# Kernel tuning notes

Hardware: AMD Instinct MI355X
Metric: run time of the kernel (lower is better)

The kernel has to match this reference:

```python
import jax, jax.numpy as jnp
import numpy as np

EPS_DIV = 1e-6    # safe_div clamp
EPS_NORM = 1e-12  # F.normalize eps
EPS_PD = 1e-6     # F.pairwise_distance eps (added to the difference)


def setup_inputs() -> dict:
    key = jax.random.key(0)
    k1, k2, k3 = jax.random.split(key, 3)
    B, N, D, C = 8, 2048, 512, 8192
    x = jax.random.normal(k1, (B, N, D), dtype=jnp.float32)
    W = jax.random.normal(k2, (D, D), dtype=jnp.float32) * (1.0 / np.sqrt(D))
    codebook = jax.random.normal(k3, (C, D), dtype=jnp.float32)
    return {"x": x, "W": W, "codebook": codebook}


def reference(x, W, codebook):
    sg = jax.lax.stop_gradient
    # implicit codebook = Linear(dim, dim, bias=False)(codebook)  -> codebook @ W^T
    imp = codebook @ W.T                                  # [C, D]

    lead = x.shape[:-1]
    D = x.shape[-1]
    xf = x.reshape(-1, D)                                 # [T, D]

    # nearest-neighbor search (no_grad in original): squared-dist argmin == cdist argmin
    d2 = (jnp.sum(xf * xf, axis=-1, keepdims=True)
          - 2.0 * (xf @ imp.T)
          + jnp.sum(imp * imp, axis=-1)[None, :])         # [T, C]
    indices = jnp.argmin(sg(d2), axis=-1)                 # [T]

    qf = imp[indices]                                     # [T, D] gather

    # commit loss: (pairwise_distance(x, q.detach())**2).mean(); torch adds eps to the diff
    diff = xf - sg(qf) + EPS_PD
    commit_loss = jnp.mean(jnp.sum(diff * diff, axis=-1))

    # rotation trick
    norm_x = jnp.linalg.norm(xf, axis=-1, keepdims=True)  # [T, 1]
    norm_q = jnp.linalg.norm(qf, axis=-1, keepdims=True)
    u = xf / jnp.maximum(norm_x, EPS_DIV)
    q = qf / jnp.maximum(norm_q, EPS_DIV)
    s = u + q
    w = sg(s / jnp.maximum(jnp.linalg.norm(s, axis=-1, keepdims=True), EPS_NORM))
    e = xf
    # e - 2 (e.w) w + 2 (e.u_sg) q_sg   (rank-1 products per row)
    rot = (e
           - 2.0 * jnp.sum(e * w, axis=-1, keepdims=True) * w
           + 2.0 * jnp.sum(e * sg(u), axis=-1, keepdims=True) * sg(q))
    quantized = rot * sg(norm_q / jnp.maximum(norm_x, EPS_DIV))

    quantized = quantized.reshape(*lead, D)
    indices = indices.reshape(*lead)
    return quantized, indices, commit_loss
```

## Files before the change

### kernel.cpp

```cpp
#include <hip/hip_runtime.h>
#include <cstdint>
#include <cstddef>

#define DD 512
#define TT 16384
#define CC 8192
#define SPLITC 64
#define EPS_DIV 1e-6f
#define EPS_NORM 1e-12f
#define EPS_PD 1e-6f

typedef _Float16 half8 __attribute__((ext_vector_type(8)));
typedef _Float16 half4 __attribute__((ext_vector_type(4)));
typedef float floatx4 __attribute__((ext_vector_type(4)));

#define GLDS16(g, l) __builtin_amdgcn_global_load_lds( \
    (const __attribute__((address_space(1))) void*)(g), \
    (__attribute__((address_space(3))) void*)(l), 16, 0, 0)

__global__ __launch_bounds__(128) void k_split(const float* __restrict__ src,
                                               _Float16* __restrict__ dst) {
  const int row = blockIdx.x;
  const int col = threadIdx.x * 4;
  float4 v = *(const float4*)(src + (size_t)row * DD + col);
  half4 h, l;
  h.x = (_Float16)v.x; l.x = (_Float16)(v.x - (float)h.x);
  h.y = (_Float16)v.y; l.y = (_Float16)(v.y - (float)h.y);
  h.z = (_Float16)v.z; l.z = (_Float16)(v.z - (float)h.z);
  h.w = (_Float16)v.w; l.w = (_Float16)(v.w - (float)h.w);
  *(half4*)(dst + (size_t)row * 1024 + col) = h;
  *(half4*)(dst + (size_t)row * 1024 + 512 + col) = l;
}

__global__ __launch_bounds__(128) void k_cast16(const float* __restrict__ src,
                                                _Float16* __restrict__ dst) {
  const int row = blockIdx.x;
  const int col = threadIdx.x * 4;
  float4 v = *(const float4*)(src + (size_t)row * DD + col);
  half4 h;
  h.x = (_Float16)v.x; h.y = (_Float16)v.y;
  h.z = (_Float16)v.z; h.w = (_Float16)v.w;
  *(half4*)(dst + (size_t)row * DD + col) = h;
}

__global__ __launch_bounds__(256) void k_gemm_mfma(
    const _Float16* __restrict__ cbs, const _Float16* __restrict__ Ws,
    float* __restrict__ imp, _Float16* __restrict__ ih) {
  __shared__ __align__(16) char smem[65536];
  const int tid = threadIdx.x;
  const int w = tid >> 6, lane = tid & 63;
  const int quad = lane >> 4, l15 = lane & 15;
  const int wm = (w & 1) * 64, wn = (w >> 1) * 64;
  const int c0 = blockIdx.x * 128;
  const int n0 = blockIdx.y * 128;

  const int srow8 = lane >> 3;
  const int scol = ((lane & 7) ^ srow8) << 3;
  size_t arow[4], brow[4];
#pragma unroll
  for (int j = 0; j < 4; ++j) {
    arow[j] = (size_t)(c0 + j * 32 + w * 8 + srow8) * 1024 + scol;
    brow[j] = (size_t)(n0 + j * 32 + w * 8 + srow8) * 1024 + scol;
  }
  int aoff[4], boff[4];
#pragma unroll
  for (int i = 0; i < 4; ++i) {
    aoff[i] = ((wm + i * 16 + l15) * 64 + ((quad ^ (l15 & 7)) << 3)) * 2;
    boff[i] = ((wn + i * 16 + l15) * 64 + ((quad ^ (l15 & 7)) << 3)) * 2;
  }

  auto stage = [&](int buf, int ak, int bk) {
    char* ab = smem + buf * 32768;
    char* bb = ab + 16384;
#pragma unroll
    for (int j = 0; j < 4; ++j) {
      GLDS16(cbs + arow[j] + ak, (_Float16*)ab + (j * 32 + w * 8) * 64);
      GLDS16(Ws  + brow[j] + bk, (_Float16*)bb + (j * 32 + w * 8) * 64);
    }
  };

  floatx4 acc[4][4] = {};
  stage(0, 0, 0);
#pragma unroll 2
  for (int it = 0; it < 24; ++it) {
    __syncthreads();
    if (it < 23) {
      const int n = it + 1;
      const int p = n >> 3, kk = n & 7;
      const int ak = ((p == 2) ? 512 : 0) + kk * 64;
      const int bk = ((p == 1) ? 512 : 0) + kk * 64;
      stage(n & 1, ak, bk);
    }
    const char* ab = smem + (it & 1) * 32768;
    const char* bb = ab + 16384;
#pragma unroll
    for (int ks = 0; ks < 2; ++ks) {
      const int kx = ks * 64;
      half8 a[4], b[4];
#pragma unroll
      for (int mi = 0; mi < 4; ++mi)
        a[mi] = *(const half8*)(ab + (aoff[mi] ^ kx));
#pragma unroll
      for (int ni = 0; ni < 4; ++ni)
        b[ni] = *(const half8*)(bb + (boff[ni] ^ kx));
#pragma unroll
      for (int mi = 0; mi < 4; ++mi)
#pragma unroll
        for (int ni = 0; ni < 4; ++ni)
          acc[mi][ni] = __builtin_amdgcn_mfma_f32_16x16x32_f16(
              a[mi], b[ni], acc[mi][ni], 0, 0, 0);
    }
  }
#pragma unroll
  for (int mi = 0; mi < 4; ++mi)
#pragma unroll
    for (int r = 0; r < 4; ++r) {
      const int c = c0 + wm + mi * 16 + quad * 4 + r;
#pragma unroll
      for (int ni = 0; ni < 4; ++ni) {
        const int d = n0 + wn + ni * 16 + l15;
        const float v = acc[mi][ni][r];
        imp[(size_t)c * DD + d] = v;
        ih[(size_t)c * DD + d] = (_Float16)v;
      }
    }
}

__global__ __launch_bounds__(256) void k_row_norm2(
    const float* __restrict__ imp, float* __restrict__ cnorm) {
  const int lane = threadIdx.x & 63;
  const int row = blockIdx.x * 4 + (threadIdx.x >> 6);
  const float* p = imp + (size_t)row * DD + lane * 8;
  float4 a = *(const float4*)p;
  float4 b = *(const float4*)(p + 4);
  float s = a.x * a.x + a.y * a.y + a.z * a.z + a.w * a.w +
            b.x * b.x + b.y * b.y + b.z * b.z + b.w * b.w;
#pragma unroll
  for (int m = 1; m < 64; m <<= 1) s += __shfl_xor(s, m);
  if (lane == 0) cnorm[row] = s;
}

__global__ __launch_bounds__(256) void k_dist_top2(
    const _Float16* __restrict__ xh, const _Float16* __restrict__ ih,
    const float* __restrict__ cnorm,
    float* __restrict__ bval, int* __restrict__ bidx) {
  __shared__ __align__(16) char smem[65536];
  const int tid = threadIdx.x;
  const int w = tid >> 6, lane = tid & 63;
  const int quad = lane >> 4, l15 = lane & 15;
  const int wm = (w & 1) * 64, wn = (w >> 1) * 64;
  const int r0 = blockIdx.x * 128;
  const int c0 = blockIdx.y * 128;

  const int srow8 = lane >> 3;
  const int scol = ((lane & 7) ^ srow8) << 3;
  size_t arow[4], brow[4];
#pragma unroll
  for (int j = 0; j < 4; ++j) {
    arow[j] = (size_t)(r0 + j * 32 + w * 8 + srow8) * DD + scol;
    brow[j] = (size_t)(c0 + j * 32 + w * 8 + srow8) * DD + scol;
  }
  int aoff[4], boff[4];
#pragma unroll
  for (int i = 0; i < 4; ++i) {
    aoff[i] = ((wm + i * 16 + l15) * 64 + ((quad ^ (l15 & 7)) << 3)) * 2;
    boff[i] = ((wn + i * 16 + l15) * 64 + ((quad ^ (l15 & 7)) << 3)) * 2;
  }

  auto stage = [&](int buf, int k0) {
    char* ab = smem + buf * 32768;
    char* bb = ab + 16384;
#pragma unroll
    for (int j = 0; j < 4; ++j) {
      GLDS16(xh + arow[j] + k0, (_Float16*)ab + (j * 32 + w * 8) * 64);
      GLDS16(ih + brow[j] + k0, (_Float16*)bb + (j * 32 + w * 8) * 64);
    }
  };

  floatx4 acc[4][4] = {};
  stage(0, 0);
#pragma unroll
  for (int kk = 0; kk < 8; ++kk) {
    __syncthreads();
    if (kk < 7) stage((kk + 1) & 1, (kk + 1) * 64);
    const char* ab = smem + (kk & 1) * 32768;
    const char* bb = ab + 16384;
#pragma unroll
    for (int ks = 0; ks < 2; ++ks) {
      const int kx = ks * 64;
      half8 a[4], b[4];
#pragma unroll
      for (int mi = 0; mi < 4; ++mi)
        a[mi] = *(const half8*)(ab + (aoff[mi] ^ kx));
#pragma unroll
      for (int ni = 0; ni < 4; ++ni)
        b[ni] = *(const half8*)(bb + (boff[ni] ^ kx));
#pragma unroll
      for (int mi = 0; mi < 4; ++mi)
#pragma unroll
        for (int ni = 0; ni < 4; ++ni)
          acc[mi][ni] = __builtin_amdgcn_mfma_f32_16x16x32_f16(
              a[mi], b[ni], acc[mi][ni], 0, 0, 0);
    }
  }
  float best[16];
  int bsti[16];
#pragma unroll
  for (int mi = 0; mi < 4; ++mi)
#pragma unroll
    for (int r = 0; r < 4; ++r) {
      const int s = mi * 4 + r;
      best[s] = 3.4e38f; bsti[s] = 0;
#pragma unroll
      for (int ni = 0; ni < 4; ++ni) {
        const int c = c0 + wn + ni * 16 + l15;
        const float v = fmaf(-2.0f, acc[mi][ni][r], cnorm[c]);
        if (v < best[s]) { best[s] = v; bsti[s] = c; }
      }
    }
  __syncthreads();
  float* rv = (float*)smem;
  int* ri = (int*)(smem + 16896);
  const int e = (w >> 1) * 16 + l15;
#pragma unroll
  for (int mi = 0; mi < 4; ++mi)
#pragma unroll
    for (int r = 0; r < 4; ++r) {
      const int row = wm + mi * 16 + quad * 4 + r;
      rv[row * 33 + e] = best[mi * 4 + r];
      ri[row * 33 + e] = bsti[mi * 4 + r];
    }
  __syncthreads();
  if (tid < 128) {
    float v1 = 3.4e38f, v2 = 3.4e38f;
    int i1 = 0x7fffffff, i2 = 0x7fffffff;
#pragma unroll
    for (int t = 0; t < 32; ++t) {
      const float v = rv[tid * 33 + t];
      const int i = ri[tid * 33 + t];
      if (v < v1 || (v == v1 && i < i1)) {
        v2 = v1; i2 = i1; v1 = v; i1 = i;
      } else if (v < v2 || (v == v2 && i < i2)) {
        v2 = v; i2 = i;
      }
    }
    const size_t o = ((size_t)blockIdx.y * TT + r0 + tid) * 2;
    bval[o] = v1; bval[o + 1] = v2;
    bidx[o] = i1; bidx[o + 1] = i2;
  }
}

__global__ __launch_bounds__(256) void k_epilogue(
    const float* __restrict__ x, const float* __restrict__ imp,
    const float* __restrict__ cnorm,
    const float* __restrict__ bval, const int* __restrict__ bidx,
    float* __restrict__ outq, float* __restrict__ outidx,
    float* __restrict__ rloss) {
  const int lane = threadIdx.x & 63;
  const int row = blockIdx.x * 4 + (threadIdx.x >> 6);
  const size_t o = ((size_t)lane * TT + row) * 2;
  float v1 = bval[o], v2 = bval[o + 1];
  int i1 = bidx[o], i2 = bidx[o + 1];
#pragma unroll
  for (int m = 1; m < 64; m <<= 1) {
    const float w1 = __shfl_xor(v1, m), w2 = __shfl_xor(v2, m);
    const int j1 = __shfl_xor(i1, m), j2 = __shfl_xor(i2, m);
    if (w1 < v1 || (w1 == v1 && j1 < i1)) {
      if (v1 < w2 || (v1 == w2 && i1 < j2)) { v2 = v1; i2 = i1; }
      else { v2 = w2; i2 = j2; }
      v1 = w1; i1 = j1;
    } else {
      if (w1 < v2 || (w1 == v2 && j1 < i2)) { v2 = w1; i2 = j1; }
    }
  }
  const float* xr = x + (size_t)row * DD + lane * 8;
  float e[8], qa[8], qb[8];
  *(float4*)&e[0] = *(const float4*)xr;
  *(float4*)&e[4] = *(const float4*)(xr + 4);
  const float* q1p = imp + (size_t)i1 * DD + lane * 8;
  const float* q2p = imp + (size_t)i2 * DD + lane * 8;
  *(float4*)&qa[0] = *(const float4*)q1p;
  *(float4*)&qa[4] = *(const float4*)(q1p + 4);
  *(float4*)&qb[0] = *(const float4*)q2p;
  *(float4*)&qb[4] = *(const float4*)(q2p + 4);
  float d1 = 0.f, d2 = 0.f;
#pragma unroll
  for (int k = 0; k < 8; ++k) {
    d1 = fmaf(e[k], qa[k], d1);
    d2 = fmaf(e[k], qb[k], d2);
  }
#pragma unroll
  for (int m = 1; m < 64; m <<= 1) {
    d1 += __shfl_xor(d1, m);
    d2 += __shfl_xor(d2, m);
  }
  const float s1 = fmaf(-2.0f, d1, cnorm[i1]);
  const float s2 = fmaf(-2.0f, d2, cnorm[i2]);
  const bool use2 = (s2 < s1) || (s2 == s1 && i2 < i1);
  const int idx = use2 ? i2 : i1;
  float q[8];
#pragma unroll
  for (int k = 0; k < 8; ++k) q[k] = use2 ? qb[k] : qa[k];

  float xx = 0.f, qq = 0.f, xq = 0.f, cl = 0.f;
#pragma unroll
  for (int k = 0; k < 8; ++k) {
    xx = fmaf(e[k], e[k], xx);
    qq = fmaf(q[k], q[k], qq);
    xq = fmaf(e[k], q[k], xq);
    float d = e[k] - q[k] + EPS_PD;
    cl = fmaf(d, d, cl);
  }
#pragma unroll
  for (int m = 1; m < 64; m <<= 1) {
    xx += __shfl_xor(xx, m);
    qq += __shfl_xor(qq, m);
    xq += __shfl_xor(xq, m);
    cl += __shfl_xor(cl, m);
  }
  const float nx = sqrtf(xx), nq = sqrtf(qq);
  const float dx = fmaxf(nx, EPS_DIV), dq = fmaxf(nq, EPS_DIV);
  const float uu = xx / (dx * dx);
  const float qq2 = qq / (dq * dq);
  const float uq = xq / (dx * dq);
  const float ss = uu + qq2 + 2.0f * uq;
  const float dn = fmaxf(sqrtf(ss), EPS_NORM);
  const float es = xx / dx + xq / dq;
  const float a = 2.0f * es / (dn * dn);
  const float b = 2.0f * (xx / dx);
  const float scale = nq / dx;

  float ov[8];
#pragma unroll
  for (int k = 0; k < 8; ++k) {
    const float qp = q[k] / dq;
    const float sk = e[k] / dx + qp;
    ov[k] = (e[k] - a * sk + b * qp) * scale;
  }
  float* op = outq + (size_t)row * DD + lane * 8;
  *(float4*)op = *(const float4*)&ov[0];
  *(float4*)(op + 4) = *(const float4*)&ov[4];
  if (lane == 0) {
    outidx[row] = (float)idx;
    rloss[row] = cl;
  }
}

__global__ __launch_bounds__(256) void k_loss_final(
    const float* __restrict__ rloss, float* __restrict__ out) {
  __shared__ double red[256];
  const int tid = threadIdx.x;
  double s = 0.0;
  for (int i = tid; i < TT; i += 256) s += (double)rloss[i];
  red[tid] = s;
  __syncthreads();
  for (int st = 128; st > 0; st >>= 1) {
    if (tid < st) red[tid] += red[tid + st];
    __syncthreads();
  }
  if (tid == 0) out[0] = (float)(red[0] / (double)TT);
}

extern "C" void kernel_launch(void* const* d_in, const int* in_sizes, int n_in,
                              void* d_out, int out_size, void* d_ws, size_t ws_size,
                              hipStream_t stream) {
  const float* x  = (const float*)d_in[0];
  const float* W  = (const float*)d_in[1];
  const float* cb = (const float*)d_in[2];
  float* out = (float*)d_out;

  float* imp = (float*)d_ws;
  _Float16* ih = (_Float16*)(imp + (size_t)CC * DD);
  _Float16* cbs = ih + (size_t)CC * DD;
  _Float16* xh = cbs;
  _Float16* Ws = cbs + (size_t)CC * 1024;
  float* cnorm = (float*)(Ws + (size_t)DD * 1024);
  float* bval  = cnorm + CC;
  int*   bidx  = (int*)(bval + (size_t)SPLITC * TT * 2);
  float* rloss = (float*)(bidx + (size_t)SPLITC * TT * 2);

  float* out_q    = out;
  float* out_idx  = out + (size_t)TT * DD;
  float* out_loss = out_idx + TT;

  k_split<<<CC, 128, 0, stream>>>(cb, cbs);
  k_split<<<DD, 128, 0, stream>>>(W, Ws);
  k_gemm_mfma<<<dim3(CC / 128, DD / 128), 256, 0, stream>>>(cbs, Ws, imp, ih);
  k_row_norm2<<<CC / 4, 256, 0, stream>>>(imp, cnorm);
  k_cast16<<<TT, 128, 0, stream>>>(x, xh);
  k_dist_top2<<<dim3(TT / 128, SPLITC), 256, 0, stream>>>(xh, ih, cnorm, bval, bidx);
  k_epilogue<<<TT / 4, 256, 0, stream>>>(x, imp, cnorm, bval, bidx, out_q, out_idx, rloss);
  k_loss_final<<<1, 256, 0, stream>>>(rloss, out_loss);
}
```

Baseline: 374.7 us.

## Enlarge distance GEMM tile to 256x256 with 4-stage async LDS pipeline

Reworks the distance/top-2 kernel to use 512-thread blocks computing 256x256 tiles, which halves the number of column splits and doubles operand reuse per global load. K is consumed in 32-wide steps through a 4-deep ring of LDS buffers fed by global_load_lds, using explicit vmcnt waits, raw barriers and setprio around the MFMA block. The per-row reduction gets an XOR-swizzled LDS layout, and the work is split across two threads joined by a shuffle. The epilogue masks lanes beyond the smaller split count. The kernel needs 128KB of LDS and more registers per thread (8x4 accumulators), which may limit occupancy.

```diff
diff --git a/kernel.cpp b/kernel.cpp
--- a/kernel.cpp
+++ b/kernel.cpp
@@ -5,7 +5,7 @@
 #define DD 512
 #define TT 16384
 #define CC 8192
-#define SPLITC 64
+#define SPLITC 32
 #define EPS_DIV 1e-6f
 #define EPS_NORM 1e-12f
 #define EPS_PD 1e-6f
@@ -140,113 +140,142 @@
   if (lane == 0) cnorm[row] = s;
 }
 
-__global__ __launch_bounds__(256) void k_dist_top2(
+__global__ __launch_bounds__(512, 2) void k_dist_top2(
     const _Float16* __restrict__ xh, const _Float16* __restrict__ ih,
     const float* __restrict__ cnorm,
     float* __restrict__ bval, int* __restrict__ bidx) {
-  __shared__ __align__(16) char smem[65536];
+  __shared__ __align__(16) char smem[131072];
   const int tid = threadIdx.x;
   const int w = tid >> 6, lane = tid & 63;
   const int quad = lane >> 4, l15 = lane & 15;
-  const int wm = (w & 1) * 64, wn = (w >> 1) * 64;
-  const int r0 = blockIdx.x * 128;
-  const int c0 = blockIdx.y * 128;
-
-  const int srow8 = lane >> 3;
-  const int scol = ((lane & 7) ^ srow8) << 3;
-  size_t arow[4], brow[4];
-#pragma unroll
-  for (int j = 0; j < 4; ++j) {
-    arow[j] = (size_t)(r0 + j * 32 + w * 8 + srow8) * DD + scol;
-    brow[j] = (size_t)(c0 + j * 32 + w * 8 + srow8) * DD + scol;
-  }
-  int aoff[4], boff[4];
-#pragma unroll
-  for (int i = 0; i < 4; ++i) {
-    aoff[i] = ((wm + i * 16 + l15) * 64 + ((quad ^ (l15 & 7)) << 3)) * 2;
-    boff[i] = ((wn + i * 16 + l15) * 64 + ((quad ^ (l15 & 7)) << 3)) * 2;
-  }
-
-  auto stage = [&](int buf, int k0) {
-    char* ab = smem + buf * 32768;
-    char* bb = ab + 16384;
-#pragma unroll
-    for (int j = 0; j < 4; ++j) {
-      GLDS16(xh + arow[j] + k0, (_Float16*)ab + (j * 32 + w * 8) * 64);
-      GLDS16(ih + brow[j] + k0, (_Float16*)bb + (j * 32 + w * 8) * 64);
-    }
+  const int wr = w >> 2, wc = w & 3;
+  const int r0 = blockIdx.x * 256;
+  const int c0 = blockIdx.y * 256;
+
+  const int rloc = lane >> 2;
+  const int chunk = (lane & 3) ^ (rloc & 3) ^ ((rloc >> 2) & 3);
+  const _Float16* pA0 = xh + (size_t)(r0 + w * 32 + rloc) * DD + chunk * 8;
+  const _Float16* pA1 = pA0 + (size_t)16 * DD;
+  const _Float16* pB0 = ih + (size_t)(c0 + w * 32 + rloc) * DD + chunk * 8;
+  const _Float16* pB1 = pB0 + (size_t)16 * DD;
+  const int ldsA0 = (w * 32) * 64;
+  const int ldsA1 = ldsA0 + 16 * 64;
+  const int ldsB0 = 16384 + ldsA0;
+  const int ldsB1 = 16384 + ldsA1;
+
+  const int slot = (quad ^ (l15 & 3) ^ ((l15 >> 2) & 3)) << 4;
+  int aoff[8], boff[4];
+#pragma unroll
+  for (int mi = 0; mi < 8; ++mi)
+    aoff[mi] = (wr * 128 + mi * 16 + l15) * 64 + slot;
+#pragma unroll
+  for (int ni = 0; ni < 4; ++ni)
+    boff[ni] = 16384 + (wc * 64 + ni * 16 + l15) * 64 + slot;
+
+  float cn[4];
+#pragma unroll
+  for (int ni = 0; ni < 4; ++ni)
+    cn[ni] = cnorm[c0 + wc * 64 + ni * 16 + l15];
+
+  floatx4 acc[8][4] = {};
+
+  auto STAGE = [&](int t) {
+    char* base = smem + (t & 3) * 32768;
+    const size_t ko = (size_t)(t * 32);
+    GLDS16(pA0 + ko, base + ldsA0);
+    GLDS16(pA1 + ko, base + ldsA1);
+    GLDS16(pB0 + ko, base + ldsB0);
+    GLDS16(pB1 + ko, base + ldsB1);
   };
-
-  floatx4 acc[4][4] = {};
-  stage(0, 0);
-#pragma unroll
-  for (int kk = 0; kk < 8; ++kk) {
-    __syncthreads();
-    if (kk < 7) stage((kk + 1) & 1, (kk + 1) * 64);
-    const char* ab = smem + (kk & 1) * 32768;
-    const char* bb = ab + 16384;
-#pragma unroll
-    for (int ks = 0; ks < 2; ++ks) {
-      const int kx = ks * 64;
-      half8 a[4], b[4];
-#pragma unroll
-      for (int mi = 0; mi < 4; ++mi)
-        a[mi] = *(const half8*)(ab + (aoff[mi] ^ kx));
+  auto COMPUTE = [&](int t) {
+    const char* ab = smem + (t & 3) * 32768;
+    half8 a[8], b[4];
+#pragma unroll
+    for (int mi = 0; mi < 8; ++mi) a[mi] = *(const half8*)(ab + aoff[mi]);
+#pragma unroll
+    for (int ni = 0; ni < 4; ++ni) b[ni] = *(const half8*)(ab + boff[ni]);
+    asm volatile("s_waitcnt lgkmcnt(0)" ::: "memory");
+    __builtin_amdgcn_sched_barrier(0);
+    __builtin_amdgcn_s_barrier();
+    __builtin_amdgcn_sched_barrier(0);
+    __builtin_amdgcn_s_setprio(1);
+#pragma unroll
+    for (int mi = 0; mi < 8; ++mi)
 #pragma unroll
       for (int ni = 0; ni < 4; ++ni)
-        b[ni] = *(const half8*)(bb + (boff[ni] ^ kx));
-#pragma unroll
-      for (int mi = 0; mi < 4; ++mi)
-#pragma unroll
-        for (int ni = 0; ni < 4; ++ni)
-          acc[mi][ni] = __builtin_amdgcn_mfma_f32_16x16x32_f16(
-              a[mi], b[ni], acc[mi][ni], 0, 0, 0);
-    }
-  }
-  float best[16];
-  int bsti[16];
-#pragma unroll
-  for (int mi = 0; mi < 4; ++mi)
-#pragma unroll
-    for (int r = 0; r < 4; ++r) {
-      const int s = mi * 4 + r;
-      best[s] = 3.4e38f; bsti[s] = 0;
-#pragma unroll
-      for (int ni = 0; ni < 4; ++ni) {
-        const int c = c0 + wn + ni * 16 + l15;
-        const float v = fmaf(-2.0f, acc[mi][ni][r], cnorm[c]);
-        if (v < best[s]) { best[s] = v; bsti[s] = c; }
-      }
-    }
+        acc[mi][ni] = __builtin_amdgcn_mfma_f32_16x16x32_f16(
+            a[mi], b[ni], acc[mi][ni], 0, 0, 0);
+    __builtin_amdgcn_s_setprio(0);
+  };
+
+  STAGE(0); STAGE(1); STAGE(2);
+#pragma unroll 1
+  for (int t = 0; t < 13; ++t) {
+    STAGE(t + 3);
+    asm volatile("s_waitcnt vmcnt(12)" ::: "memory");
+    __builtin_amdgcn_s_barrier();
+    __builtin_amdgcn_sched_barrier(0);
+    COMPUTE(t);
+  }
+  asm volatile("s_waitcnt vmcnt(8)" ::: "memory");
+  __builtin_amdgcn_s_barrier();
+  __builtin_amdgcn_sched_barrier(0);
+  COMPUTE(13);
+  asm volatile("s_waitcnt vmcnt(4)" ::: "memory");
+  __builtin_amdgcn_s_barrier();
+  __builtin_amdgcn_sched_barrier(0);
+  COMPUTE(14);
+  asm volatile("s_waitcnt vmcnt(0)" ::: "memory");
+  __builtin_amdgcn_s_barrier();
+  __builtin_amdgcn_sched_barrier(0);
+  COMPUTE(15);
+
   __syncthreads();
   float* rv = (float*)smem;
-  int* ri = (int*)(smem + 16896);
-  const int e = (w >> 1) * 16 + l15;
-#pragma unroll
-  for (int mi = 0; mi < 4; ++mi)
+  int* ri = (int*)(smem + 65536);
+#pragma unroll
+  for (int mi = 0; mi < 8; ++mi)
 #pragma unroll
     for (int r = 0; r < 4; ++r) {
-      const int row = wm + mi * 16 + quad * 4 + r;
-      rv[row * 33 + e] = best[mi * 4 + r];
-      ri[row * 33 + e] = bsti[mi * 4 + r];
+      const int row = wr * 128 + mi * 16 + quad * 4 + r;
+      float bv = 3.4e38f; int bi = 0x7fffffff;
+#pragma unroll
+      for (int ni = 0; ni < 4; ++ni) {
+        const float v = fmaf(-2.0f, acc[mi][ni][r], cn[ni]);
+        const int c = c0 + wc * 64 + ni * 16 + l15;
+        if (v < bv) { bv = v; bi = c; }
+      }
+      const int e = wc * 16 + l15;
+      const int col = e ^ (row & 31);
+      rv[row * 64 + col] = bv;
+      ri[row * 64 + col] = bi;
     }
   __syncthreads();
-  if (tid < 128) {
+  {
+    const int row = tid >> 1, h = tid & 1;
     float v1 = 3.4e38f, v2 = 3.4e38f;
     int i1 = 0x7fffffff, i2 = 0x7fffffff;
 #pragma unroll
-    for (int t = 0; t < 32; ++t) {
-      const float v = rv[tid * 33 + t];
-      const int i = ri[tid * 33 + t];
-      if (v < v1 || (v == v1 && i < i1)) {
-        v2 = v1; i2 = i1; v1 = v; i1 = i;
-      } else if (v < v2 || (v == v2 && i < i2)) {
-        v2 = v; i2 = i;
-      }
-    }
-    const size_t o = ((size_t)blockIdx.y * TT + r0 + tid) * 2;
-    bval[o] = v1; bval[o + 1] = v2;
-    bidx[o] = i1; bidx[o + 1] = i2;
+    for (int j = 0; j < 32; ++j) {
+      const int e = h * 32 + j;
+      const int col = e ^ (row & 31);
+      const float v = rv[row * 64 + col];
+      const int i = ri[row * 64 + col];
+      if (v < v1 || (v == v1 && i < i1)) { v2 = v1; i2 = i1; v1 = v; i1 = i; }
+      else if (v < v2 || (v == v2 && i < i2)) { v2 = v; i2 = i; }
+    }
+    const float w1 = __shfl_xor(v1, 1), w2 = __shfl_xor(v2, 1);
+    const int j1 = __shfl_xor(i1, 1), j2 = __shfl_xor(i2, 1);
+    if (w1 < v1 || (w1 == v1 && j1 < i1)) {
+      if (v1 < w2 || (v1 == w2 && i1 < j2)) { v2 = v1; i2 = i1; }
+      else { v2 = w2; i2 = j2; }
+      v1 = w1; i1 = j1;
+    } else if (w1 < v2 || (w1 == v2 && j1 < i2)) { v2 = w1; i2 = j1; }
+    if (h == 0) {
+      const size_t o = ((size_t)blockIdx.y * TT + r0 + row) * 2;
+      bval[o] = v1; bval[o + 1] = v2;
+      bidx[o] = i1; bidx[o + 1] = i2;
+    }
   }
 }
 
@@ -258,9 +287,13 @@
     float* __restrict__ rloss) {
   const int lane = threadIdx.x & 63;
   const int row = blockIdx.x * 4 + (threadIdx.x >> 6);
-  const size_t o = ((size_t)lane * TT + row) * 2;
-  float v1 = bval[o], v2 = bval[o + 1];
-  int i1 = bidx[o], i2 = bidx[o + 1];
+  float v1 = 3.4e38f, v2 = 3.4e38f;
+  int i1 = 0x7fffffff, i2 = 0x7fffffff;
+  if (lane < SPLITC) {
+    const size_t o = ((size_t)lane * TT + row) * 2;
+    v1 = bval[o]; v2 = bval[o + 1];
+    i1 = bidx[o]; i2 = bidx[o + 1];
+  }
 #pragma unroll
   for (int m = 1; m < 64; m <<= 1) {
     const float w1 = __shfl_xor(v1, m), w2 = __shfl_xor(v2, m);
@@ -388,7 +421,7 @@
   k_gemm_mfma<<<dim3(CC / 128, DD / 128), 256, 0, stream>>>(cbs, Ws, imp, ih);
   k_row_norm2<<<CC / 4, 256, 0, stream>>>(imp, cnorm);
   k_cast16<<<TT, 128, 0, stream>>>(x, xh);
-  k_dist_top2<<<dim3(TT / 128, SPLITC), 256, 0, stream>>>(xh, ih, cnorm, bval, bidx);
+  k_dist_top2<<<dim3(TT / 256, CC / 256), 512, 0, stream>>>(xh, ih, cnorm, bval, bidx);
   k_epilogue<<<TT / 4, 256, 0, stream>>>(x, imp, cnorm, bval, bidx, out_q, out_idx, rloss);
   k_loss_final<<<1, 256, 0, stream>>>(rloss, out_loss);
 }
```

After: 343.3 us. 8.4% less time.
